# Performance work log

Hardware: AMD Instinct MI355X
Metric: run time of the kernel (lower is better)

The kernel has to match this reference:

```python
import jax, jax.numpy as jnp
import numpy as np

DIM = 2048
HEADS = 16
HEAD_DIM = DIM // HEADS


def setup_inputs() -> dict:
    key = jax.random.key(0)
    ks = jax.random.split(key, 9)
    B, S = 1, 4096
    X = jax.random.normal(ks[0], (B, S, DIM), dtype=jnp.float32)
    sc = 1.0 / np.sqrt(DIM)
    Wq = jax.random.normal(ks[1], (DIM, DIM), dtype=jnp.float32) * sc
    bq = jax.random.normal(ks[2], (DIM,), dtype=jnp.float32) * 0.01
    Wk = jax.random.normal(ks[3], (DIM, DIM), dtype=jnp.float32) * sc
    bk = jax.random.normal(ks[4], (DIM,), dtype=jnp.float32) * 0.01
    Wv = jax.random.normal(ks[5], (DIM, DIM), dtype=jnp.float32) * sc
    bv = jax.random.normal(ks[6], (DIM,), dtype=jnp.float32) * 0.01
    Wo = jax.random.normal(ks[7], (DIM, DIM), dtype=jnp.float32) * sc
    bo = jax.random.normal(ks[8], (DIM,), dtype=jnp.float32) * 0.01
    return {"X": X, "Wq": Wq, "bq": bq, "Wk": Wk, "bk": bk,
            "Wv": Wv, "bv": bv, "Wo": Wo, "bo": bo, "is_causal": 1}


def reference(X, Wq, bq, Wk, bk, Wv, bv, Wo, bo, is_causal):
    B, S, _ = X.shape
    # torch nn.Linear: y = x @ W^T + b
    Q = (X @ Wq.T + bq).reshape(B, S, HEADS, HEAD_DIM).transpose(0, 2, 1, 3)
    K = (X @ Wk.T + bk).reshape(B, S, HEADS, HEAD_DIM).transpose(0, 2, 1, 3)
    V = (X @ Wv.T + bv).reshape(B, S, HEADS, HEAD_DIM).transpose(0, 2, 1, 3)
    scores = jnp.einsum('bhqd,bhkd->bhqk', Q, K) / np.sqrt(HEAD_DIM)  # [B,H,S,S]
    if is_causal:
        causal = jnp.tril(jnp.ones((S, S), dtype=bool))
        scores = jnp.where(causal, scores, -jnp.inf)
    attn = jax.nn.softmax(scores, axis=-1)
    # dropout_rate = 0 (eval) -> identity
    Out = jnp.einsum('bhqk,bhkd->bhqd', attn, V)
    Out = Out.transpose(0, 2, 1, 3).reshape(B, S, DIM)
    return Out @ Wo.T + bo
```

## Files before the change

kernel.cpp:

```cpp
#include <hip/hip_runtime.h>
#include <hip/hip_bf16.h>

typedef unsigned short u16;
typedef __attribute__((ext_vector_type(8))) short short8;
typedef __attribute__((ext_vector_type(4))) short short4v;
typedef __attribute__((ext_vector_type(4))) float floatx4;

constexpr int SEQ = 4096;
constexpr int DM  = 2048;
constexpr int NH  = 16;
constexpr int HD  = 128;

__device__ inline u16 f2b(float f) {
    __hip_bfloat16 h = __float2bfloat16(f);
    return *reinterpret_cast<u16*>(&h);
}
__device__ inline float b2f(u16 u) {
    __hip_bfloat16 h = *reinterpret_cast<__hip_bfloat16*>(&u);
    return __bfloat162float(h);
}

__device__ __forceinline__ void async_copy16(const u16* g, u16* lds_base) {
    __builtin_amdgcn_global_load_lds(
        (const __attribute__((address_space(1))) unsigned int*)g,
        (__attribute__((address_space(3))) unsigned int*)lds_base,
        16, 0, 0);
}

__global__ void detect_dtype(const u16* __restrict__ X, int* __restrict__ flag) {
    __shared__ int cnt;
    if (threadIdx.x == 0) cnt = 0;
    __syncthreads();
    int local = 0;
    for (int i = threadIdx.x; i < 4096; i += 256) {
        int e = (X[i] >> 7) & 0xFF;
        if (e >= 0x3C && e <= 0x8D) local++;
    }
    atomicAdd(&cnt, local);
    __syncthreads();
    if (threadIdx.x == 0) *flag = (cnt >= 3890) ? 1 : 0;
}

struct ConvArgs {
    const void* src[9];
    unsigned long long dstoff[9];
    int n[9];
};
__global__ void convert_all(ConvArgs a, u16* __restrict__ base,
                            const int* __restrict__ flag) {
    const int t = blockIdx.y;
    const int n = a.n[t];
    const int i = (blockIdx.x * blockDim.x + threadIdx.x) * 8;
    if (i >= n) return;
    u16* out = base + a.dstoff[t];
    if (*flag) {
        *(short8*)&out[i] = *(const short8*)&((const u16*)a.src[t])[i];
    } else {
        const float* p = (const float*)a.src[t];
        u16 tmp[8];
#pragma unroll
        for (int j = 0; j < 8; j++) tmp[j] = f2b(p[i + j]);
        *(short8*)&out[i] = *(const short8*)tmp;
    }
}

__device__ __forceinline__ void gemm256_core(
    const u16* __restrict__ A, const u16* __restrict__ W,
    int m0, int n0, floatx4 (&acc)[8][4])
{
    __shared__ __align__(16) u16 As[2][16384];
    __shared__ __align__(16) u16 Bs[2][16384];
    constexpr int K  = DM;
    constexpr int NT = K / 64;

    const int tid  = threadIdx.x;
    const int lane = tid & 63;
    const int w    = tid >> 6;
    const int qm   = lane & 15;
    const int quad = lane >> 4;
    const int wm   = (w >> 2) * 128;
    const int wn   = (w & 3) * 64;

    const int srow = tid >> 3;
    const int scol = ((tid & 7) ^ (srow & 7)) * 8;

    const int fo0 = (quad ^ (qm & 7)) * 8;
    const int fo1 = fo0 ^ 32;

    const u16* Ag = A + (size_t)(m0 + srow) * K + scol;
    const u16* Wg = W + (size_t)(n0 + srow) * K + scol;

#define STG_A(s, b, k0) async_copy16(Ag + (size_t)(s) * 64 * K + (k0), &As[b][(s) * 4096 + w * 512])
#define STG_B(s, b, k0) async_copy16(Wg + (size_t)(s) * 64 * K + (k0), &Bs[b][(s) * 4096 + w * 512])

#pragma unroll
    for (int i = 0; i < 8; ++i)
#pragma unroll
        for (int j = 0; j < 4; ++j) acc[i][j] = floatx4{0.f, 0.f, 0.f, 0.f};

#pragma unroll
    for (int s = 0; s < 4; ++s) STG_A(s, 0, 0);
#pragma unroll
    for (int s = 0; s < 4; ++s) STG_B(s, 0, 0);

    short8 bf[4][2];

    for (int t = 0; t < NT; ++t) {
        const int cb = t & 1, nb = cb ^ 1;
        const int kn = (t + 1) * 64;
        const u16* Ac = As[cb];
        const u16* Bc = Bs[cb];
        const bool more = (t + 1 < NT);
#pragma unroll
        for (int q = 0; q < 4; ++q) {
            if (more) {
                if      (q == 0) { STG_A(0, nb, kn); STG_A(1, nb, kn); }
                else if (q == 1) { STG_A(2, nb, kn); STG_A(3, nb, kn); }
                else if (q == 2) { STG_B(0, nb, kn); STG_B(1, nb, kn); }
                else             { STG_B(2, nb, kn); STG_B(3, nb, kn); }
            }
            short8 a00, a01, a10, a11;
            if (q == 0) {
                if (more) asm volatile("s_waitcnt vmcnt(2)" ::: "memory");
                else      asm volatile("s_waitcnt vmcnt(0)" ::: "memory");
                __builtin_amdgcn_s_barrier();
#pragma unroll
                for (int nt = 0; nt < 4; ++nt) {
                    const int br = wn + nt * 16 + qm;
                    bf[nt][0] = *(const short8*)&Bc[br * 64 + fo0];
                    bf[nt][1] = *(const short8*)&Bc[br * 64 + fo1];
                }
                const int r0 = wm + qm, r1 = wm + 16 + qm;
                a00 = *(const short8*)&Ac[r0 * 64 + fo0];
                a01 = *(const short8*)&Ac[r0 * 64 + fo1];
                a10 = *(const short8*)&Ac[r1 * 64 + fo0];
                a11 = *(const short8*)&Ac[r1 * 64 + fo1];
            } else {
                const int r0 = wm + (2 * q) * 16 + qm, r1 = r0 + 16;
                a00 = *(const short8*)&Ac[r0 * 64 + fo0];
                a01 = *(const short8*)&Ac[r0 * 64 + fo1];
                a10 = *(const short8*)&Ac[r1 * 64 + fo0];
                a11 = *(const short8*)&Ac[r1 * 64 + fo1];
                __builtin_amdgcn_s_barrier();
            }
            asm volatile("s_waitcnt lgkmcnt(0)" ::: "memory");
            __builtin_amdgcn_sched_barrier(0);
            __builtin_amdgcn_s_setprio(1);
#pragma unroll
            for (int nt = 0; nt < 4; ++nt) {
                acc[2*q][nt]   = __builtin_amdgcn_mfma_f32_16x16x32_bf16(a00, bf[nt][0], acc[2*q][nt], 0, 0, 0);
                acc[2*q][nt]   = __builtin_amdgcn_mfma_f32_16x16x32_bf16(a01, bf[nt][1], acc[2*q][nt], 0, 0, 0);
                acc[2*q+1][nt] = __builtin_amdgcn_mfma_f32_16x16x32_bf16(a10, bf[nt][0], acc[2*q+1][nt], 0, 0, 0);
                acc[2*q+1][nt] = __builtin_amdgcn_mfma_f32_16x16x32_bf16(a11, bf[nt][1], acc[2*q+1][nt], 0, 0, 0);
            }
            __builtin_amdgcn_s_setprio(0);
            __builtin_amdgcn_s_barrier();
        }
    }
#undef STG_A
#undef STG_B
}

__launch_bounds__(512, 2)
__global__ void gemm_qkv(const u16* __restrict__ A, const u16* __restrict__ W,
                         const u16* __restrict__ bias,
                         u16* __restrict__ Qb, u16* __restrict__ Kb,
                         u16* __restrict__ VtG) {
    const int m0 = blockIdx.y * 256;
    const int n0 = blockIdx.x * 256;
    floatx4 acc[8][4];
    gemm256_core(A, W, m0, n0, acc);

    const int tid  = threadIdx.x;
    const int lane = tid & 63;
    const int w    = tid >> 6;
    const int qm   = lane & 15;
    const int quad = lane >> 4;
    const int wm   = (w >> 2) * 128;
    const int wn   = (w & 3) * 64;

    const int buf = n0 >> 11;
    if (buf < 2) {
        u16* Y = (buf == 0) ? Qb : Kb;
#pragma unroll
        for (int nt = 0; nt < 4; ++nt) {
            const int gcol = n0 + wn + nt * 16 + qm;
            const int col  = gcol & 2047;
            const float bv = b2f(bias[gcol]);
#pragma unroll
            for (int mt = 0; mt < 8; ++mt) {
                const int rbase = m0 + wm + mt * 16 + quad * 4;
#pragma unroll
                for (int r = 0; r < 4; ++r)
                    Y[(size_t)(rbase + r) * DM + col] = f2b(acc[mt][nt][r] + bv);
            }
        }
    } else {
#pragma unroll
        for (int nt = 0; nt < 4; ++nt) {
            const int gcol = n0 + wn + nt * 16 + qm;
            const int col  = gcol & 2047;
            const float bv = b2f(bias[gcol]);
#pragma unroll
            for (int mt = 0; mt < 8; ++mt) {
                const int rbase = m0 + wm + mt * 16 + quad * 4;
                u16 tmp[4];
#pragma unroll
                for (int r = 0; r < 4; ++r)
                    tmp[r] = f2b(acc[mt][nt][r] + bv);
                *(short4v*)&VtG[(size_t)col * SEQ + rbase] = *(const short4v*)tmp;
            }
        }
    }
}

__launch_bounds__(512, 2)
__global__ void gemm_out(const u16* __restrict__ A, const u16* __restrict__ W,
                         const u16* __restrict__ bias, void* __restrict__ out,
                         const int* __restrict__ flag) {
    const int m0 = blockIdx.y * 256;
    const int n0 = blockIdx.x * 256;
    floatx4 acc[8][4];
    gemm256_core(A, W, m0, n0, acc);

    const int tid  = threadIdx.x;
    const int lane = tid & 63;
    const int w    = tid >> 6;
    const int qm   = lane & 15;
    const int quad = lane >> 4;
    const int wm   = (w >> 2) * 128;
    const int wn   = (w & 3) * 64;
    const int N    = DM;

    const int f = *flag;
#pragma unroll
    for (int nt = 0; nt < 4; ++nt) {
        const int col = n0 + wn + nt * 16 + qm;
        const float bv = b2f(bias[col]);
#pragma unroll
        for (int mt = 0; mt < 8; ++mt) {
            const int rbase = m0 + wm + mt * 16 + quad * 4;
#pragma unroll
            for (int r = 0; r < 4; ++r) {
                const float v = acc[mt][nt][r] + bv;
                if (f) ((u16*)out)[(size_t)(rbase + r) * N + col] = f2b(v);
                else   ((float*)out)[(size_t)(rbase + r) * N + col] = v;
            }
        }
    }
}

__launch_bounds__(512)
__global__ void attn_kernel(const u16* __restrict__ Q, const u16* __restrict__ K,
                            const u16* __restrict__ Vt, u16* __restrict__ O,
                            const int* __restrict__ is_causal_p) {
    __shared__ __align__(16) u16 Ks[64][136];
    __shared__ __align__(16) u16 Vts[128][72];
    __shared__ __align__(16) u16 Pb[8][16][72];

    const int tid  = threadIdx.x;
    const int lane = tid & 63;
    const int w    = tid >> 6;
    const int qm   = lane & 15;
    const int quad = lane >> 4;
    const int xt   = ((blockIdx.y >> 3) & 1) ? (gridDim.x - 1 - blockIdx.x)
                                             : blockIdx.x;
    const int q0   = xt * 128;
    const int h    = blockIdx.y;
    const int causal = *is_causal_p;
    const float scale = 0.08838834764831845f;
    const float SHIFT = 16.0f;

    short8 qf[4];
    {
        const u16* qptr = Q + (size_t)(q0 + w * 16 + qm) * DM + h * HD;
#pragma unroll
        for (int kc = 0; kc < 4; kc++)
            qf[kc] = *(const short8*)&qptr[kc * 32 + quad * 8];
    }

    floatx4 o[8];
#pragma unroll
    for (int dt = 0; dt < 8; dt++) o[dt] = floatx4{0.f, 0.f, 0.f, 0.f};
    float l_part[4] = {0.f, 0.f, 0.f, 0.f};

    const int jend = causal ? (q0 + 128) : SEQ;

    const int kr0 = tid >> 4;
    const int kc8 = (tid & 15) * 8;
    const int vd0 = tid >> 3;
    const int vc8 = (tid & 7) * 8;

    short8 kreg[2], vreg[2];
#pragma unroll
    for (int p = 0; p < 2; p++) {
        kreg[p] = *(const short8*)&K[(size_t)(kr0 + p * 32) * DM + h * HD + kc8];
        vreg[p] = *(const short8*)&Vt[(size_t)(h * HD + vd0 + p * 64) * SEQ + vc8];
    }

    for (int j0 = 0; j0 < jend; j0 += 64) {
#pragma unroll
        for (int p = 0; p < 2; p++) {
            *(short8*)&Ks[kr0 + p * 32][kc8] = kreg[p];
            *(short8*)&Vts[vd0 + p * 64][vc8] = vreg[p];
        }
        __syncthreads();

        const int jn = (j0 + 64 < jend) ? j0 + 64 : 0;
#pragma unroll
        for (int p = 0; p < 2; p++) {
            kreg[p] = *(const short8*)&K[(size_t)(jn + kr0 + p * 32) * DM + h * HD + kc8];
            vreg[p] = *(const short8*)&Vt[(size_t)(h * HD + vd0 + p * 64) * SEQ + jn + vc8];
        }

        floatx4 s[4];
#pragma unroll
        for (int nt = 0; nt < 4; nt++) s[nt] = floatx4{0.f, 0.f, 0.f, 0.f};
#pragma unroll
        for (int kc = 0; kc < 4; kc++)
#pragma unroll
            for (int nt = 0; nt < 4; nt++) {
                short8 b = *(const short8*)&Ks[nt * 16 + qm][kc * 32 + quad * 8];
                s[nt] = __builtin_amdgcn_mfma_f32_16x16x32_bf16(qf[kc], b, s[nt], 0, 0, 0);
            }

        const bool mask = causal && (j0 + 64 > q0 + w * 16);
#pragma unroll
        for (int r = 0; r < 4; r++) {
            const int qg = q0 + w * 16 + quad * 4 + r;
#pragma unroll
            for (int nt = 0; nt < 4; nt++) {
                float v = fmaf(s[nt][r], scale, -SHIFT);
                if (mask && (j0 + nt * 16 + qm > qg)) v = -1e30f;
                const float p = __expf(v);
                l_part[r] += p;
                Pb[w][quad * 4 + r][nt * 16 + qm] = f2b(p);
            }
        }
        asm volatile("s_waitcnt lgkmcnt(0)" ::: "memory");

#pragma unroll
        for (int kc = 0; kc < 2; kc++) {
            short8 pf = *(const short8*)&Pb[w][qm][kc * 32 + quad * 8];
#pragma unroll
            for (int dt = 0; dt < 8; dt++) {
                short8 b = *(const short8*)&Vts[dt * 16 + qm][kc * 32 + quad * 8];
                o[dt] = __builtin_amdgcn_mfma_f32_16x16x32_bf16(pf, b, o[dt], 0, 0, 0);
            }
        }
        __syncthreads();
    }

#pragma unroll
    for (int r = 0; r < 4; r++) {
        float l = l_part[r];
#pragma unroll
        for (int off = 8; off >= 1; off >>= 1)
            l += __shfl_xor(l, off, 64);
        const float inv = 1.0f / l;
        const int qg = q0 + w * 16 + quad * 4 + r;
#pragma unroll
        for (int dt = 0; dt < 8; dt++) {
            const int d = h * HD + dt * 16 + qm;
            O[(size_t)qg * DM + d] = f2b(o[dt][r] * inv);
        }
    }
}

extern "C" void kernel_launch(void* const* d_in, const int* in_sizes, int n_in,
                              void* d_out, int out_size, void* d_ws, size_t ws_size,
                              hipStream_t stream) {
    const int* isc = (const int*)d_in[9];

    int* flag = (int*)d_ws;
    u16* base = (u16*)((char*)d_ws + 256);

    const int NX = SEQ * DM;
    const int NW = DM * DM;
    const int NB = DM;

    unsigned long long off = 0;
    const unsigned long long oXc   = off; off += NX;
    const unsigned long long oWall = off; off += 3ull * NW;
    const unsigned long long oWo   = off; off += NW;
    const unsigned long long oBall = off; off += 3ull * NB;
    const unsigned long long oBo   = off; off += NB;
    const unsigned long long oQ    = off; off += NX;
    const unsigned long long oK    = off; off += NX;
    const unsigned long long oVt   = off; off += NX;
    const unsigned long long oA    = off; off += NX;

    detect_dtype<<<1, 256, 0, stream>>>((const u16*)d_in[0], flag);

    ConvArgs ca;
    const unsigned long long dsts[9] = {oXc, oWall, oBall, oWall + NW, oBall + NB,
                                        oWall + 2ull * NW, oBall + 2ull * NB, oWo, oBo};
    for (int i = 0; i < 9; i++) {
        ca.src[i] = d_in[i];
        ca.dstoff[i] = dsts[i];
        ca.n[i] = in_sizes[i];
    }
    convert_all<<<dim3(NX / 8 / 256, 9), 256, 0, stream>>>(ca, base, flag);

    gemm_qkv<<<dim3(3 * DM / 256, SEQ / 256), 512, 0, stream>>>(
        base + oXc, base + oWall, base + oBall,
        base + oQ, base + oK, base + oVt);

    attn_kernel<<<dim3(SEQ / 128, NH), 512, 0, stream>>>(
        base + oQ, base + oK, base + oVt, base + oA, isc);

    gemm_out<<<dim3(DM / 256, SEQ / 256), 512, 0, stream>>>(
        base + oA, base + oWo, base + oBo, d_out, flag);
}
```

Before: 502.5 us.

## Deepen GEMM prefetch to two stages and cut barriers per K-step

The 256x256 GEMM core now preloads two K-tiles before the loop and refills each LDS buffer with tile t+2 as soon as it has been consumed. B-tile refills start after the B fragments are read, and A-tile refills start at the end of the step. Barriers per K-step drop from five to two, and A-fragment LDS reads are interleaved one group ahead of the MFMA groups. The goal is to hide global-load latency and barrier stalls. The cost is higher register pressure from holding more fragments live and more outstanding vmem operations.

```diff
diff --git a/kernel.cpp b/kernel.cpp
--- a/kernel.cpp
+++ b/kernel.cpp
@@ -90,75 +90,92 @@
     const u16* Ag = A + (size_t)(m0 + srow) * K + scol;
     const u16* Wg = W + (size_t)(n0 + srow) * K + scol;
 
-#define STG_A(s, b, k0) async_copy16(Ag + (size_t)(s) * 64 * K + (k0), &As[b][(s) * 4096 + w * 512])
-#define STG_B(s, b, k0) async_copy16(Wg + (size_t)(s) * 64 * K + (k0), &Bs[b][(s) * 4096 + w * 512])
+#define STG_A4(par, k0) {                                                 \
+    async_copy16(Ag + (size_t)0 * 64 * K + (k0), &As[par][0 * 4096 + w * 512]); \
+    async_copy16(Ag + (size_t)1 * 64 * K + (k0), &As[par][1 * 4096 + w * 512]); \
+    async_copy16(Ag + (size_t)2 * 64 * K + (k0), &As[par][2 * 4096 + w * 512]); \
+    async_copy16(Ag + (size_t)3 * 64 * K + (k0), &As[par][3 * 4096 + w * 512]); }
+#define STG_B4(par, k0) {                                                 \
+    async_copy16(Wg + (size_t)0 * 64 * K + (k0), &Bs[par][0 * 4096 + w * 512]); \
+    async_copy16(Wg + (size_t)1 * 64 * K + (k0), &Bs[par][1 * 4096 + w * 512]); \
+    async_copy16(Wg + (size_t)2 * 64 * K + (k0), &Bs[par][2 * 4096 + w * 512]); \
+    async_copy16(Wg + (size_t)3 * 64 * K + (k0), &Bs[par][3 * 4096 + w * 512]); }
+
+#define RD_A(d0, d1, row) { d0 = *(const short8*)&Ac[(row) * 64 + fo0];   \
+                            d1 = *(const short8*)&Ac[(row) * 64 + fo1]; }
+
+#define MFMA_Q(q2, x00, x01, x10, x11) {                                  \
+    __builtin_amdgcn_s_setprio(1);                                        \
+    _Pragma("unroll")                                                     \
+    for (int nt = 0; nt < 4; ++nt) {                                      \
+        acc[q2][nt]     = __builtin_amdgcn_mfma_f32_16x16x32_bf16(x00, bf[nt][0], acc[q2][nt], 0, 0, 0);     \
+        acc[q2][nt]     = __builtin_amdgcn_mfma_f32_16x16x32_bf16(x01, bf[nt][1], acc[q2][nt], 0, 0, 0);     \
+        acc[q2 + 1][nt] = __builtin_amdgcn_mfma_f32_16x16x32_bf16(x10, bf[nt][0], acc[q2 + 1][nt], 0, 0, 0); \
+        acc[q2 + 1][nt] = __builtin_amdgcn_mfma_f32_16x16x32_bf16(x11, bf[nt][1], acc[q2 + 1][nt], 0, 0, 0); \
+    }                                                                     \
+    __builtin_amdgcn_s_setprio(0); }
 
 #pragma unroll
     for (int i = 0; i < 8; ++i)
 #pragma unroll
         for (int j = 0; j < 4; ++j) acc[i][j] = floatx4{0.f, 0.f, 0.f, 0.f};
 
-#pragma unroll
-    for (int s = 0; s < 4; ++s) STG_A(s, 0, 0);
-#pragma unroll
-    for (int s = 0; s < 4; ++s) STG_B(s, 0, 0);
-
-    short8 bf[4][2];
+    STG_A4(0, 0);
+    STG_B4(0, 0);
+    STG_A4(1, 64);
+    STG_B4(1, 64);
+    asm volatile("s_waitcnt vmcnt(8)" ::: "memory");
+    __builtin_amdgcn_s_barrier();
+    asm volatile("" ::: "memory");
 
     for (int t = 0; t < NT; ++t) {
-        const int cb = t & 1, nb = cb ^ 1;
-        const int kn = (t + 1) * 64;
-        const u16* Ac = As[cb];
-        const u16* Bc = Bs[cb];
-        const bool more = (t + 1 < NT);
-#pragma unroll
-        for (int q = 0; q < 4; ++q) {
-            if (more) {
-                if      (q == 0) { STG_A(0, nb, kn); STG_A(1, nb, kn); }
-                else if (q == 1) { STG_A(2, nb, kn); STG_A(3, nb, kn); }
-                else if (q == 2) { STG_B(0, nb, kn); STG_B(1, nb, kn); }
-                else             { STG_B(2, nb, kn); STG_B(3, nb, kn); }
-            }
-            short8 a00, a01, a10, a11;
-            if (q == 0) {
-                if (more) asm volatile("s_waitcnt vmcnt(2)" ::: "memory");
-                else      asm volatile("s_waitcnt vmcnt(0)" ::: "memory");
-                __builtin_amdgcn_s_barrier();
-#pragma unroll
-                for (int nt = 0; nt < 4; ++nt) {
-                    const int br = wn + nt * 16 + qm;
-                    bf[nt][0] = *(const short8*)&Bc[br * 64 + fo0];
-                    bf[nt][1] = *(const short8*)&Bc[br * 64 + fo1];
-                }
-                const int r0 = wm + qm, r1 = wm + 16 + qm;
-                a00 = *(const short8*)&Ac[r0 * 64 + fo0];
-                a01 = *(const short8*)&Ac[r0 * 64 + fo1];
-                a10 = *(const short8*)&Ac[r1 * 64 + fo0];
-                a11 = *(const short8*)&Ac[r1 * 64 + fo1];
-            } else {
-                const int r0 = wm + (2 * q) * 16 + qm, r1 = r0 + 16;
-                a00 = *(const short8*)&Ac[r0 * 64 + fo0];
-                a01 = *(const short8*)&Ac[r0 * 64 + fo1];
-                a10 = *(const short8*)&Ac[r1 * 64 + fo0];
-                a11 = *(const short8*)&Ac[r1 * 64 + fo1];
-                __builtin_amdgcn_s_barrier();
-            }
-            asm volatile("s_waitcnt lgkmcnt(0)" ::: "memory");
-            __builtin_amdgcn_sched_barrier(0);
-            __builtin_amdgcn_s_setprio(1);
-#pragma unroll
-            for (int nt = 0; nt < 4; ++nt) {
-                acc[2*q][nt]   = __builtin_amdgcn_mfma_f32_16x16x32_bf16(a00, bf[nt][0], acc[2*q][nt], 0, 0, 0);
-                acc[2*q][nt]   = __builtin_amdgcn_mfma_f32_16x16x32_bf16(a01, bf[nt][1], acc[2*q][nt], 0, 0, 0);
-                acc[2*q+1][nt] = __builtin_amdgcn_mfma_f32_16x16x32_bf16(a10, bf[nt][0], acc[2*q+1][nt], 0, 0, 0);
-                acc[2*q+1][nt] = __builtin_amdgcn_mfma_f32_16x16x32_bf16(a11, bf[nt][1], acc[2*q+1][nt], 0, 0, 0);
-            }
-            __builtin_amdgcn_s_setprio(0);
-            __builtin_amdgcn_s_barrier();
-        }
-    }
-#undef STG_A
-#undef STG_B
+        const int p = t & 1;
+        const u16* Ac = As[p];
+        const u16* Bc = Bs[p];
+        const bool more = (t + 2 < NT);
+        const int kf = (t + 2) * 64;
+
+        short8 bf[4][2];
+        short8 a0, a1, a2, a3, b0, b1, b2, b3;
+        short8 c0, c1, c2, c3, d0, d1, d2, d3;
+
+#pragma unroll
+        for (int nt = 0; nt < 4; ++nt) {
+            const int br = wn + nt * 16 + qm;
+            bf[nt][0] = *(const short8*)&Bc[br * 64 + fo0];
+            bf[nt][1] = *(const short8*)&Bc[br * 64 + fo1];
+        }
+        RD_A(a0, a1, wm + qm);
+        RD_A(a2, a3, wm + 16 + qm);
+        RD_A(b0, b1, wm + 32 + qm);
+        RD_A(b2, b3, wm + 48 + qm);
+        MFMA_Q(0, a0, a1, a2, a3);
+
+        RD_A(c0, c1, wm + 64 + qm);
+        RD_A(c2, c3, wm + 80 + qm);
+        MFMA_Q(2, b0, b1, b2, b3);
+
+        asm volatile("" ::: "memory");
+        __builtin_amdgcn_s_barrier();
+        asm volatile("" ::: "memory");
+        if (more) { STG_B4(p, kf); }
+
+        RD_A(d0, d1, wm + 96 + qm);
+        RD_A(d2, d3, wm + 112 + qm);
+        MFMA_Q(4, c0, c1, c2, c3);
+
+        MFMA_Q(6, d0, d1, d2, d3);
+
+        if (more) asm volatile("s_waitcnt vmcnt(4)" ::: "memory");
+        else      asm volatile("s_waitcnt vmcnt(0)" ::: "memory");
+        __builtin_amdgcn_s_barrier();
+        asm volatile("" ::: "memory");
+        if (more) { STG_A4(p, kf); }
+    }
+#undef STG_A4
+#undef STG_B4
+#undef RD_A
+#undef MFMA_Q
 }
 
 __launch_bounds__(512, 2)
```

Measured after the change: 479.7 us. -4.5%, faster.
